# Kernel optimization log

Measured on AMD Instinct MI355X. Metric: run time of the kernel, lower is better.

The kernel has to match this reference:

```python
import jax, jax.numpy as jnp
import numpy as np

N_NODES = 100000
N_EDGES = 1600000
D_IN = 128
D_OUT = 128


def setup_inputs() -> dict:
    key = jax.random.key(0)
    k1, k2, k3, k4 = jax.random.split(key, 4)
    x = jax.random.normal(k1, (N_NODES, D_IN), dtype=jnp.float32)
    edge_index = jax.random.randint(k2, (2, N_EDGES), 0, N_NODES, dtype=jnp.int64)
    # Xavier-uniform init as in the torch module
    limit = float(np.sqrt(6.0 / (D_IN + D_OUT)))
    self_weight = jax.random.uniform(k3, (D_IN, D_OUT), dtype=jnp.float32, minval=-limit, maxval=limit)
    neighbor_weight = jax.random.uniform(k4, (D_IN, D_OUT), dtype=jnp.float32, minval=-limit, maxval=limit)
    bias = jnp.zeros((D_OUT,), dtype=jnp.float32)
    return {"x": x, "edge_index": edge_index, "self_weight": self_weight,
            "neighbor_weight": neighbor_weight, "bias": bias}


def reference(x, edge_index, self_weight, neighbor_weight, bias):
    row, col = edge_index[0], edge_index[1]
    num_nodes = x.shape[0]
    # symmetric normalization: deg^-1/2 over rows, gathered per edge
    deg = jax.ops.segment_sum(jnp.ones_like(row, dtype=x.dtype), row,
                              num_segments=num_nodes)
    deg_inv_sqrt = deg ** -0.5
    norm = deg_inv_sqrt[row] * deg_inv_sqrt[col]  # [E]
    # dense transforms
    self_support = x @ self_weight                 # [N, D_OUT]
    h = x @ neighbor_weight                        # [N, D_OUT]
    # spmm: out[r] += norm_e * h[c] for each edge (r, c)
    msg = norm[:, None] * h[col]                   # [E, D_OUT]
    neighbor_support = jax.ops.segment_sum(msg, row, num_segments=num_nodes)
    return self_support + neighbor_support + bias
```

## Files before the change

### kernel.cpp

```cpp
#include <hip/hip_runtime.h>

#define N_NODES 100000
#define N_EDGES 1600000
#define D_FEAT 128
#define BUCKETS 256
#define RPB 391
#define BIN_CHUNK 8192
#define BIN_WGS ((N_EDGES + BIN_CHUNK - 1) / BIN_CHUNK)
#define CSR_CAP 12288

#define PRE_CONV_WGS (N_NODES * D_FEAT / 4 / 256)
#define PRE_WPREP_WGS 16
#define PRE_BHIST_WGS BIN_WGS
#define PRE_WGS (PRE_CONV_WGS + PRE_WPREP_WGS + PRE_BHIST_WGS)

typedef unsigned int u32;
typedef unsigned short u16;
typedef __attribute__((ext_vector_type(8))) short bf16x8;
typedef __attribute__((ext_vector_type(4))) float f32x4;

__device__ inline float bfbits2f(u32 hi) { union { u32 u; float f; } v; v.u = hi; return v.f; }
__device__ inline float bflo(u32 pair) { return bfbits2f(pair << 16); }
__device__ inline float bfhi(u32 pair) { return bfbits2f(pair & 0xFFFF0000u); }
__device__ inline u16 f2bf(float f) {
  union { float f; u32 u; } v; v.f = f;
  u32 r = v.u + 0x7FFFu + ((v.u >> 16) & 1u);
  return (u16)(r >> 16);
}
__device__ inline int clampN(int v) { return ((unsigned)v < N_NODES) ? v : 0; }

__global__ __launch_bounds__(256) void k_pre(const float4* __restrict__ x4,
                                             uint2* __restrict__ xb2,
                                             const float* __restrict__ Wself,
                                             const float* __restrict__ Wnb,
                                             u16* __restrict__ Wbf,
                                             const int* __restrict__ ei,
                                             int* __restrict__ bcnt) {
  __shared__ int h[BUCKETS];
  int b = blockIdx.x;
  int tid = threadIdx.x;
  if (b < PRE_CONV_WGS) {
    int i = b * 256 + tid;
    float4 v = x4[i];
    uint2 o;
    o.x = (u32)f2bf(v.x) | ((u32)f2bf(v.y) << 16);
    o.y = (u32)f2bf(v.z) | ((u32)f2bf(v.w) << 16);
    xb2[i] = o;
  } else if (b < PRE_CONV_WGS + PRE_WPREP_WGS) {
    int f = (b - PRE_CONV_WGS) * 256 + tid;
    int lane = f & 63, nt = (f >> 6) & 7, kk = (f >> 9) & 3, t = f >> 11;
    int q = lane >> 4, l16 = lane & 15;
    const float* W = t ? Wnb : Wself;
    int n = nt * 16 + l16;
    int k0 = (kk * 4 + q) * 8;
    u16 tmp[8];
#pragma unroll
    for (int j = 0; j < 8; j++) tmp[j] = f2bf(W[(k0 + j) * 128 + n]);
    uint4 o;
    o.x = (u32)tmp[0] | ((u32)tmp[1] << 16);
    o.y = (u32)tmp[2] | ((u32)tmp[3] << 16);
    o.z = (u32)tmp[4] | ((u32)tmp[5] << 16);
    o.w = (u32)tmp[6] | ((u32)tmp[7] << 16);
    *(uint4*)(Wbf + (long)f * 8) = o;
  } else {
    int wb = b - PRE_CONV_WGS - PRE_WPREP_WGS;
    h[tid] = 0;
    __syncthreads();
    long e0 = (long)wb * BIN_CHUNK;
#pragma unroll
    for (int j = 0; j < BIN_CHUNK / 256; j++) {
      long e = e0 + j * 256 + tid;
      if (e < N_EDGES) atomicAdd(&h[clampN(ei[e]) / RPB], 1);
    }
    __syncthreads();
    if (h[tid]) atomicAdd(&bcnt[tid], h[tid]);
  }
}

__global__ __launch_bounds__(256) void k_bscan(const int* __restrict__ bcnt,
                                               int* __restrict__ bbase,
                                               int* __restrict__ gcur) {
  __shared__ int sm[BUCKETS];
  int tid = threadIdx.x;
  int v = bcnt[tid];
  sm[tid] = v;
  __syncthreads();
  for (int off = 1; off < BUCKETS; off <<= 1) {
    int t = (tid >= off) ? sm[tid - off] : 0;
    __syncthreads();
    sm[tid] += t;
    __syncthreads();
  }
  int excl = sm[tid] - v;
  bbase[tid] = excl;
  gcur[tid] = excl;
  if (tid == BUCKETS - 1) bbase[BUCKETS] = sm[tid];
}

__global__ __launch_bounds__(256) void k_bin(const int* __restrict__ ei,
                                             int* __restrict__ gcur,
                                             u32* __restrict__ binrec) {
  __shared__ int hist[BUCKETS], pref[BUCKETS], lcur[BUCKETS], gbase[BUCKETS];
  __shared__ u32 stag[BIN_CHUNK];
  __shared__ unsigned char sbkt[BIN_CHUNK];
  int tid = threadIdx.x;
  long e0 = (long)blockIdx.x * BIN_CHUNK;
  hist[tid] = 0;
  lcur[tid] = 0;
  __syncthreads();
  int rows[BIN_CHUNK / 256];
#pragma unroll
  for (int j = 0; j < BIN_CHUNK / 256; j++) {
    long e = e0 + j * 256 + tid;
    int r = (e < N_EDGES) ? clampN(ei[e]) : -1;
    rows[j] = r;
    if (r >= 0) atomicAdd(&hist[r / RPB], 1);
  }
  __syncthreads();
  int v = hist[tid];
  pref[tid] = v;
  __syncthreads();
  for (int off = 1; off < BUCKETS; off <<= 1) {
    int t = (tid >= off) ? pref[tid - off] : 0;
    __syncthreads();
    pref[tid] += t;
    __syncthreads();
  }
  int excl = pref[tid] - v;
  gbase[tid] = atomicAdd(&gcur[tid], v);
  __syncthreads();
  pref[tid] = excl;
  __syncthreads();
#pragma unroll
  for (int j = 0; j < BIN_CHUNK / 256; j++) {
    int r = rows[j];
    if (r < 0) continue;
    long e = e0 + j * 256 + tid;
    int c = clampN(ei[N_EDGES + e]);
    int b = r / RPB;
    int rl = r - b * RPB;
    int pos = pref[b] + atomicAdd(&lcur[b], 1);
    stag[pos] = ((u32)rl << 17) | (u32)c;
    sbkt[pos] = (unsigned char)b;
  }
  __syncthreads();
  int total = pref[BUCKETS - 1] + hist[BUCKETS - 1];
  for (int i = tid; i < total; i += 256) {
    int b = sbkt[i];
    binrec[(long)gbase[b] + (i - pref[b])] = stag[i];
  }
}

__global__ __launch_bounds__(256) void k_csra(const int* __restrict__ bbase,
                                              const u32* __restrict__ binrec,
                                              int* __restrict__ deg,
                                              int* __restrict__ row_start,
                                              float* __restrict__ dis) {
  __shared__ int h[512];
  __shared__ int ps[256];
  int tid = threadIdx.x;
  int b = blockIdx.x;
  int r0 = b * RPB;
  int nrows = min(RPB, N_NODES - r0);
  int base = bbase[b];
  int cnt = bbase[b + 1] - base;
  h[tid] = 0; h[tid + 256] = 0;
  __syncthreads();
  for (int i = tid; i < cnt; i += 256) {
    u32 rec = binrec[base + i];
    atomicAdd(&h[rec >> 17], 1);
  }
  __syncthreads();
  int s0 = h[2 * tid], s1 = h[2 * tid + 1];
  ps[tid] = s0 + s1;
  __syncthreads();
  int pv = ps[tid];
  for (int off = 1; off < 256; off <<= 1) {
    int t = (tid >= off) ? ps[tid - off] : 0;
    __syncthreads();
    ps[tid] += t;
    __syncthreads();
  }
  int pexcl = ps[tid] - pv;
  if (2 * tid < nrows) {
    int r = r0 + 2 * tid;
    deg[r] = s0;
    row_start[r] = base + pexcl;
    dis[r] = s0 ? rsqrtf((float)s0) : 0.0f;
  }
  if (2 * tid + 1 < nrows) {
    int r = r0 + 2 * tid + 1;
    deg[r] = s1;
    row_start[r] = base + pexcl + s0;
    dis[r] = s1 ? rsqrtf((float)s1) : 0.0f;
  }
}

__global__ __launch_bounds__(256) void k_csrb(const int* __restrict__ bbase,
                                              const int* __restrict__ row_start,
                                              const float* __restrict__ dis,
                                              const u32* __restrict__ binrec,
                                              int2* __restrict__ cn) {
  __shared__ int cur[RPB + 1];
  __shared__ int2 win[CSR_CAP];
  int tid = threadIdx.x;
  int b = blockIdx.x;
  int r0 = b * RPB;
  int r1 = min(r0 + RPB, N_NODES);
  int base = bbase[b];
  int cnt = bbase[b + 1] - base;
  int nrows = r1 - r0;
  for (int i = tid; i < nrows; i += 256) cur[i] = row_start[r0 + i] - base;
  __syncthreads();
  if (cnt <= CSR_CAP) {
    for (int i = tid; i < cnt; i += 256) {
      u32 rec = binrec[base + i];
      int rl = rec >> 17;
      int c = rec & 0x1FFFF;
      float nrm = dis[r0 + rl] * dis[c];
      int p = atomicAdd(&cur[rl], 1);
      int2 o; o.x = c; o.y = __float_as_int(nrm);
      win[p] = o;
    }
    __syncthreads();
    for (int i = tid; i < cnt; i += 256) cn[base + i] = win[i];
  } else {
    for (int i = tid; i < cnt; i += 256) {
      u32 rec = binrec[base + i];
      int rl = rec >> 17;
      int c = rec & 0x1FFFF;
      float nrm = dis[r0 + rl] * dis[c];
      int p = base + atomicAdd(&cur[rl], 1);
      int2 o; o.x = c; o.y = __float_as_int(nrm);
      cn[p] = o;
    }
  }
}

__global__ __launch_bounds__(256) void k_agg(const int* __restrict__ row_start,
                                             const int* __restrict__ deg,
                                             const int2* __restrict__ cn,
                                             const u32* __restrict__ xb ,
                                             u32* __restrict__ aggb) {
  int wave = threadIdx.x >> 6, lane = threadIdx.x & 63;
  int r = blockIdx.x * 4 + wave;
  if (r >= N_NODES) return;
  int start = row_start[r];
  int cnt = deg[r];
  float a0 = 0.f, a1 = 0.f, b0 = 0.f, b1 = 0.f;
  int i = 0;
  for (; i + 8 <= cnt; i += 8) {
    int2 e0 = cn[start + i + 0];
    int2 e1 = cn[start + i + 1];
    int2 e2 = cn[start + i + 2];
    int2 e3 = cn[start + i + 3];
    int2 e4 = cn[start + i + 4];
    int2 e5 = cn[start + i + 5];
    int2 e6 = cn[start + i + 6];
    int2 e7 = cn[start + i + 7];
    u32 g0 = xb[(long)e0.x * 64 + lane];
    u32 g1 = xb[(long)e1.x * 64 + lane];
    u32 g2 = xb[(long)e2.x * 64 + lane];
    u32 g3 = xb[(long)e3.x * 64 + lane];
    u32 g4 = xb[(long)e4.x * 64 + lane];
    u32 g5 = xb[(long)e5.x * 64 + lane];
    u32 g6 = xb[(long)e6.x * 64 + lane];
    u32 g7 = xb[(long)e7.x * 64 + lane];
    float n0 = __int_as_float(e0.y), n1 = __int_as_float(e1.y);
    float n2 = __int_as_float(e2.y), n3 = __int_as_float(e3.y);
    float n4 = __int_as_float(e4.y), n5 = __int_as_float(e5.y);
    float n6 = __int_as_float(e6.y), n7 = __int_as_float(e7.y);
    a0 += n0 * bflo(g0); a1 += n0 * bfhi(g0);
    b0 += n1 * bflo(g1); b1 += n1 * bfhi(g1);
    a0 += n2 * bflo(g2); a1 += n2 * bfhi(g2);
    b0 += n3 * bflo(g3); b1 += n3 * bfhi(g3);
    a0 += n4 * bflo(g4); a1 += n4 * bfhi(g4);
    b0 += n5 * bflo(g5); b1 += n5 * bfhi(g5);
    a0 += n6 * bflo(g6); a1 += n6 * bfhi(g6);
    b0 += n7 * bflo(g7); b1 += n7 * bfhi(g7);
  }
  for (; i + 2 <= cnt; i += 2) {
    int2 e0 = cn[start + i];
    int2 e1 = cn[start + i + 1];
    u32 g0 = xb[(long)e0.x * 64 + lane];
    u32 g1 = xb[(long)e1.x * 64 + lane];
    float n0 = __int_as_float(e0.y), n1 = __int_as_float(e1.y);
    a0 += n0 * bflo(g0); a1 += n0 * bfhi(g0);
    b0 += n1 * bflo(g1); b1 += n1 * bfhi(g1);
  }
  if (i < cnt) {
    int2 e0 = cn[start + i];
    u32 g0 = xb[(long)e0.x * 64 + lane];
    float n0 = __int_as_float(e0.y);
    a0 += n0 * bflo(g0); a1 += n0 * bfhi(g0);
  }
  a0 += b0; a1 += b1;
  aggb[(long)r * 64 + lane] = (u32)f2bf(a0) | ((u32)f2bf(a1) << 16);
}

__global__ __launch_bounds__(256) void k_gemm(const u16* __restrict__ xb,
                                              const u16* __restrict__ aggb,
                                              const u16* __restrict__ Wbf,
                                              const float* __restrict__ bias,
                                              float* __restrict__ out) {
  int tid = threadIdx.x;
  int wave = tid >> 6, lane = tid & 63;
  int q = lane >> 4, l16 = lane & 15;
  int w0 = blockIdx.x * 128 + wave * 32;

  bf16x8 ax[2][4], ag[2][4];
#pragma unroll
  for (int mt = 0; mt < 2; mt++) {
    int node = w0 + mt * 16 + l16;
    long aoff = (long)clampN(node) * D_FEAT + q * 8;
#pragma unroll
    for (int kk = 0; kk < 4; kk++) {
      ax[mt][kk] = *(const bf16x8*)(xb + aoff + kk * 32);
      ag[mt][kk] = *(const bf16x8*)(aggb + aoff + kk * 32);
    }
  }

#pragma unroll
  for (int nt = 0; nt < 8; nt++) {
    bf16x8 bs[4], bn[4];
#pragma unroll
    for (int kk = 0; kk < 4; kk++) {
      bs[kk] = *(const bf16x8*)(Wbf + (long)(((0 * 4 + kk) * 8 + nt) * 64 + lane) * 8);
      bn[kk] = *(const bf16x8*)(Wbf + (long)(((1 * 4 + kk) * 8 + nt) * 64 + lane) * 8);
    }
    int ncol = nt * 16 + l16;
    float bv = bias[ncol];
#pragma unroll
    for (int mt = 0; mt < 2; mt++) {
      f32x4 acc = {0.f, 0.f, 0.f, 0.f};
#pragma unroll
      for (int kk = 0; kk < 4; kk++)
        acc = __builtin_amdgcn_mfma_f32_16x16x32_bf16(ax[mt][kk], bs[kk], acc, 0, 0, 0);
#pragma unroll
      for (int kk = 0; kk < 4; kk++)
        acc = __builtin_amdgcn_mfma_f32_16x16x32_bf16(ag[mt][kk], bn[kk], acc, 0, 0, 0);
#pragma unroll
      for (int reg = 0; reg < 4; reg++) {
        int node = w0 + mt * 16 + q * 4 + reg;
        if (node < N_NODES) out[(long)node * D_FEAT + ncol] = acc[reg] + bv;
      }
    }
  }
}

extern "C" void kernel_launch(void* const* d_in, const int* in_sizes, int n_in,
                              void* d_out, int out_size, void* d_ws, size_t ws_size,
                              hipStream_t stream) {
  const float* x = (const float*)d_in[0];
  const int* ei = (const int*)d_in[1];
  const float* Wself = (const float*)d_in[2];
  const float* Wnb = (const float*)d_in[3];
  const float* bias = (const float*)d_in[4];
  float* out = (float*)d_out;

  auto alignup = [](size_t v) { return (v + 511) & ~(size_t)511; };
  char* p = (char*)d_ws;
  int* deg = (int*)p;            p += alignup((size_t)N_NODES * 4);
  int* row_start = (int*)p;      p += alignup((size_t)N_NODES * 4);
  float* dis = (float*)p;        p += alignup((size_t)N_NODES * 4);
  int* bcnt = (int*)p;           p += alignup((size_t)BUCKETS * 4);
  int* bbase = (int*)p;          p += alignup((size_t)(BUCKETS + 1) * 4);
  int* gcur = (int*)p;           p += alignup((size_t)BUCKETS * 4);
  u16* Wbf = (u16*)p;            p += alignup((size_t)4096 * 8 * 2);
  int2* cn = (int2*)p;           p += alignup((size_t)N_EDGES * 8);
  u16* xb = (u16*)p;             p += alignup((size_t)N_NODES * D_FEAT * 2);
  u16* aggb = (u16*)p;           p += alignup((size_t)N_NODES * D_FEAT * 2);
  u32* binrec = (u32*)d_out;

  hipMemsetAsync(bcnt, 0, (size_t)BUCKETS * 4, stream);

  k_pre<<<PRE_WGS, 256, 0, stream>>>((const float4*)x, (uint2*)xb, Wself, Wnb, Wbf, ei, bcnt);
  k_bscan<<<1, 256, 0, stream>>>(bcnt, bbase, gcur);
  k_bin<<<BIN_WGS, 256, 0, stream>>>(ei, gcur, binrec);
  k_csra<<<BUCKETS, 256, 0, stream>>>(bbase, binrec, deg, row_start, dis);
  k_csrb<<<BUCKETS, 256, 0, stream>>>(bbase, row_start, dis, binrec, cn);
  k_agg<<<(N_NODES + 3) / 4, 256, 0, stream>>>(row_start, deg, cn, (const u32*)xb, (u32*)aggb);
  k_gemm<<<(N_NODES + 127) / 128, 256, 0, stream>>>(xb, aggb, Wbf, bias, out);
}
```

Baseline: 268.3 us.

## Split each wave into two half-waves processing alternate edges with 8-byte gathers

The aggregation kernel now has each wave handle four rows in sequence. Within a row, the two 32-lane halves take alternating edges, each lane gathers 8 bytes (four bf16 features), and the halves are combined with a cross-lane shuffle before the write. The aim is to keep more independent gathers in flight per wave and to use wider, more efficient loads. In exchange, tail edges are padded with zero weights (wasted loads for low-degree rows), the per-row loop runs serially, and the grid is smaller.

```diff
diff --git a/kernel.cpp b/kernel.cpp
--- a/kernel.cpp
+++ b/kernel.cpp
@@ -13,6 +13,8 @@
 #define PRE_WPREP_WGS 16
 #define PRE_BHIST_WGS BIN_WGS
 #define PRE_WGS (PRE_CONV_WGS + PRE_WPREP_WGS + PRE_BHIST_WGS)
+
+#define AGG_WGS ((N_NODES + 15) / 16)
 
 typedef unsigned int u32;
 typedef unsigned short u16;
@@ -241,61 +243,48 @@
                                              const int* __restrict__ deg,
                                              const int2* __restrict__ cn,
                                              const u32* __restrict__ xb ,
-                                             u32* __restrict__ aggb) {
+                                             uint2* __restrict__ aggb2) {
   int wave = threadIdx.x >> 6, lane = threadIdx.x & 63;
-  int r = blockIdx.x * 4 + wave;
-  if (r >= N_NODES) return;
-  int start = row_start[r];
-  int cnt = deg[r];
-  float a0 = 0.f, a1 = 0.f, b0 = 0.f, b1 = 0.f;
-  int i = 0;
-  for (; i + 8 <= cnt; i += 8) {
-    int2 e0 = cn[start + i + 0];
-    int2 e1 = cn[start + i + 1];
-    int2 e2 = cn[start + i + 2];
-    int2 e3 = cn[start + i + 3];
-    int2 e4 = cn[start + i + 4];
-    int2 e5 = cn[start + i + 5];
-    int2 e6 = cn[start + i + 6];
-    int2 e7 = cn[start + i + 7];
-    u32 g0 = xb[(long)e0.x * 64 + lane];
-    u32 g1 = xb[(long)e1.x * 64 + lane];
-    u32 g2 = xb[(long)e2.x * 64 + lane];
-    u32 g3 = xb[(long)e3.x * 64 + lane];
-    u32 g4 = xb[(long)e4.x * 64 + lane];
-    u32 g5 = xb[(long)e5.x * 64 + lane];
-    u32 g6 = xb[(long)e6.x * 64 + lane];
-    u32 g7 = xb[(long)e7.x * 64 + lane];
-    float n0 = __int_as_float(e0.y), n1 = __int_as_float(e1.y);
-    float n2 = __int_as_float(e2.y), n3 = __int_as_float(e3.y);
-    float n4 = __int_as_float(e4.y), n5 = __int_as_float(e5.y);
-    float n6 = __int_as_float(e6.y), n7 = __int_as_float(e7.y);
-    a0 += n0 * bflo(g0); a1 += n0 * bfhi(g0);
-    b0 += n1 * bflo(g1); b1 += n1 * bfhi(g1);
-    a0 += n2 * bflo(g2); a1 += n2 * bfhi(g2);
-    b0 += n3 * bflo(g3); b1 += n3 * bfhi(g3);
-    a0 += n4 * bflo(g4); a1 += n4 * bfhi(g4);
-    b0 += n5 * bflo(g5); b1 += n5 * bfhi(g5);
-    a0 += n6 * bflo(g6); a1 += n6 * bfhi(g6);
-    b0 += n7 * bflo(g7); b1 += n7 * bfhi(g7);
-  }
-  for (; i + 2 <= cnt; i += 2) {
-    int2 e0 = cn[start + i];
-    int2 e1 = cn[start + i + 1];
-    u32 g0 = xb[(long)e0.x * 64 + lane];
-    u32 g1 = xb[(long)e1.x * 64 + lane];
-    float n0 = __int_as_float(e0.y), n1 = __int_as_float(e1.y);
-    a0 += n0 * bflo(g0); a1 += n0 * bfhi(g0);
-    b0 += n1 * bflo(g1); b1 += n1 * bfhi(g1);
-  }
-  if (i < cnt) {
-    int2 e0 = cn[start + i];
-    u32 g0 = xb[(long)e0.x * 64 + lane];
-    float n0 = __int_as_float(e0.y);
-    a0 += n0 * bflo(g0); a1 += n0 * bfhi(g0);
-  }
-  a0 += b0; a1 += b1;
-  aggb[(long)r * 64 + lane] = (u32)f2bf(a0) | ((u32)f2bf(a1) << 16);
+  int half = lane >> 5, l32 = lane & 31;
+  int rbase = (blockIdx.x * 4 + wave) * 4;
+#pragma unroll 1
+  for (int rr = 0; rr < 4; rr++) {
+    int r = rbase + rr;
+    if (r >= N_NODES) return;
+    int start = row_start[r];
+    int cnt = deg[r];
+    float a0 = 0.f, a1 = 0.f, a2 = 0.f, a3 = 0.f;
+    for (int i = 0; i < cnt; i += 16) {
+      int2 e[8];
+      uint2 g[8];
+#pragma unroll
+      for (int j = 0; j < 8; j++) {
+        int idx = i + 2 * j + half;
+        e[j] = cn[start + ((idx < cnt) ? idx : 0)];
+      }
+#pragma unroll
+      for (int j = 0; j < 8; j++)
+        g[j] = *(const uint2*)(xb + (long)e[j].x * 64 + 2 * l32);
+#pragma unroll
+      for (int j = 0; j < 8; j++) {
+        int idx = i + 2 * j + half;
+        float n = (idx < cnt) ? __int_as_float(e[j].y) : 0.0f;
+        a0 += n * bflo(g[j].x); a1 += n * bfhi(g[j].x);
+        a2 += n * bflo(g[j].y); a3 += n * bfhi(g[j].y);
+      }
+    }
+    float u0 = __shfl(a0, l32 + 32);
+    float u1 = __shfl(a1, l32 + 32);
+    float u2 = __shfl(a2, l32 + 32);
+    float u3 = __shfl(a3, l32 + 32);
+    if (half == 0) {
+      a0 += u0; a1 += u1; a2 += u2; a3 += u3;
+      uint2 o;
+      o.x = (u32)f2bf(a0) | ((u32)f2bf(a1) << 16);
+      o.y = (u32)f2bf(a2) | ((u32)f2bf(a3) << 16);
+      aggb2[(long)r * 32 + l32] = o;
+    }
+  }
 }
 
 __global__ __launch_bounds__(256) void k_gemm(const u16* __restrict__ xb,
@@ -379,6 +368,6 @@
   k_bin<<<BIN_WGS, 256, 0, stream>>>(ei, gcur, binrec);
   k_csra<<<BUCKETS, 256, 0, stream>>>(bbase, binrec, deg, row_start, dis);
   k_csrb<<<BUCKETS, 256, 0, stream>>>(bbase, row_start, dis, binrec, cn);
-  k_agg<<<(N_NODES + 3) / 4, 256, 0, stream>>>(row_start, deg, cn, (const u32*)xb, (u32*)aggb);
+  k_agg<<<AGG_WGS, 256, 0, stream>>>(row_start, deg, cn, (const u32*)xb, (uint2*)aggb);
   k_gemm<<<(N_NODES + 127) / 128, 256, 0, stream>>>(xb, aggb, Wbf, bias, out);
 }
```

After: 282.3 us. 1.05x slower.
